# Kernel optimization log

Measured on AMD Instinct MI355X. Metric: run time of the kernel, lower is better.

## Reference

```python
import jax, jax.numpy as jnp
import numpy as np


def setup_inputs() -> dict:
    key = jax.random.key(0)
    k1, k2, k3 = jax.random.split(key, 3)
    B, D = 16, 512
    lengths = np.array([1024 + 64 * i for i in range(B)], dtype=np.int64)  # ragged lens, max 1984
    N = int(lengths.sum())  # 24064 packed tokens
    h = jax.random.normal(k1, (N, D), dtype=jnp.float32)
    W = jax.random.normal(k2, (D, D), dtype=jnp.float32) / np.sqrt(D)
    b = jax.random.normal(k3, (D,), dtype=jnp.float32) * 0.01
    return {
        "h": h,
        "W": W,
        "b": b,
        "text_len_tensor": jnp.asarray(lengths),
        "max_len": int(lengths.max()),
    }


def reference(h, W, b, text_len_tensor, max_len):
    # h: [N, D] packed utterance features; text_len_tensor: [B] segment lengths.
    N, D = h.shape
    x = h @ W.T + b  # nn.Linear
    # Segment start offsets and padded gather indices [B, Lmax]
    offsets = jnp.concatenate(
        [jnp.zeros((1,), text_len_tensor.dtype), jnp.cumsum(text_len_tensor)[:-1]]
    )
    pos = jnp.arange(max_len)
    idx = offsets[:, None] + pos[None, :]
    mask = pos[None, :] < text_len_tensor[:, None]  # [B, Lmax] valid-token mask
    idx_c = jnp.clip(idx, 0, N - 1)
    z = h[idx_c] * mask[..., None]  # padded raw features  [B, Lmax, D]
    y = x[idx_c] * mask[..., None]  # padded projected     [B, Lmax, D]
    # Per-segment attention: scores[i, j] = z_i . y_j within each segment
    scores = jnp.einsum('bld,bmd->blm', z, y)
    scores = jnp.where(mask[:, None, :], scores, -1e9)  # mask invalid keys
    probs = jax.nn.softmax(scores, axis=-1)
    out = jnp.einsum('blm,bmd->bld', probs, z) * mask[..., None]
    # Scatter padded result back to packed layout (padding rows contribute zeros)
    ret = jnp.zeros_like(h).at[idx_c.reshape(-1)].add(out.reshape(-1, D))
    return ret
```

## Files before the change

### kernel.cpp

```cpp
#include <hip/hip_runtime.h>
#include <math.h>

#define D 512
#define AS1 __attribute__((address_space(1)))
#define AS3 __attribute__((address_space(3)))

typedef _Float16 f16x8 __attribute__((ext_vector_type(8)));
typedef float f32x4 __attribute__((ext_vector_type(4)));

__global__ __launch_bounds__(256) void transpose_kernel(
    const float* __restrict__ h, _Float16* __restrict__ zTb, int N)
{
    __shared__ float tile[64][65];
    const int t0 = blockIdx.x * 64;
    const int d0 = blockIdx.y * 64;
    const int tid = threadIdx.x;
    const int r0 = tid >> 4;
    const int c0 = (tid & 15) * 4;
    #pragma unroll
    for (int k = 0; k < 4; k++) {
        int r = r0 + k * 16;
        float4 v = *(const float4*)(h + (size_t)(t0 + r) * D + d0 + c0);
        tile[r][c0] = v.x; tile[r][c0+1] = v.y; tile[r][c0+2] = v.z; tile[r][c0+3] = v.w;
    }
    __syncthreads();
    const int g = (t0 >> 5) + (c0 >> 5);
    const int kk = c0 & 31;
    const int kg = kk >> 3;
    const int sub = kk & 7;
    #pragma unroll
    for (int k = 0; k < 4; k++) {
        int dd = d0 + r0 + k * 16;
        int kks = ((kg + (dd >> 1)) & 3) * 8 + sub;
        union { _Float16 hh[4]; uint2 u2; } pk;
        #pragma unroll
        for (int i = 0; i < 4; i++) pk.hh[i] = (_Float16)tile[c0 + i][r0 + k * 16];
        *(uint2*)(zTb + (size_t)g * 16384 + dd * 32 + kks) = pk.u2;
    }
}

__global__ __launch_bounds__(256) void linear_mfma(
    const float* __restrict__ h, const float* __restrict__ W,
    const float* __restrict__ bias, _Float16* __restrict__ x16, int N)
{
    __shared__ _Float16 sA[128 * 72];
    __shared__ _Float16 sB[128 * 72];
    const int tid  = threadIdx.x;
    const int m0 = blockIdx.x * 128;
    const int n0 = blockIdx.y * 128;
    const int wave = tid >> 6, lane = tid & 63;
    const int l15 = lane & 15, quad = lane >> 4;
    const int wm = (wave >> 1) * 64, wn = (wave & 1) * 64;

    f32x4 acc[4][4];
    #pragma unroll
    for (int mi = 0; mi < 4; mi++)
        #pragma unroll
        for (int ni = 0; ni < 4; ni++) acc[mi][ni] = (f32x4){0.f,0.f,0.f,0.f};

    for (int k0 = 0; k0 < D; k0 += 64) {
        __syncthreads();
        #pragma unroll
        for (int i = 0; i < 8; i++) {
            int idx = tid + 256 * i;
            int row = idx >> 4;
            int c4  = (idx & 15) * 4;
            float4 va = *(const float4*)(h + (size_t)(m0 + row) * D + k0 + c4);
            float4 vb = *(const float4*)(W + (size_t)(n0 + row) * D + k0 + c4);
            union { _Float16 hh[4]; uint2 u2; } pa, pb;
            pa.hh[0] = (_Float16)va.x; pa.hh[1] = (_Float16)va.y;
            pa.hh[2] = (_Float16)va.z; pa.hh[3] = (_Float16)va.w;
            pb.hh[0] = (_Float16)vb.x; pb.hh[1] = (_Float16)vb.y;
            pb.hh[2] = (_Float16)vb.z; pb.hh[3] = (_Float16)vb.w;
            *(uint2*)(sA + row * 72 + c4) = pa.u2;
            *(uint2*)(sB + row * 72 + c4) = pb.u2;
        }
        __syncthreads();
        #pragma unroll
        for (int kc = 0; kc < 2; kc++) {
            f16x8 a[4], b[4];
            #pragma unroll
            for (int mi = 0; mi < 4; mi++)
                a[mi] = *(const f16x8*)(sA + (wm + mi*16 + l15)*72 + kc*32 + quad*8);
            #pragma unroll
            for (int ni = 0; ni < 4; ni++)
                b[ni] = *(const f16x8*)(sB + (wn + ni*16 + l15)*72 + kc*32 + quad*8);
            #pragma unroll
            for (int mi = 0; mi < 4; mi++)
                #pragma unroll
                for (int ni = 0; ni < 4; ni++)
                    acc[mi][ni] = __builtin_amdgcn_mfma_f32_16x16x32_f16(a[mi], b[ni], acc[mi][ni], 0, 0, 0);
        }
    }
    float bv[4];
    #pragma unroll
    for (int ni = 0; ni < 4; ni++) bv[ni] = bias[n0 + wn + ni*16 + l15];
    #pragma unroll
    for (int mi = 0; mi < 4; mi++)
        #pragma unroll
        for (int ni = 0; ni < 4; ni++)
            #pragma unroll
            for (int r = 0; r < 4; r++) {
                int row = m0 + wm + mi*16 + quad*4 + r;
                x16[(size_t)row * D + n0 + wn + ni*16 + l15] = (_Float16)(acc[mi][ni][r] + bv[ni]);
            }
}

__global__ __launch_bounds__(256, 2) void attn8_kernel(
    const float* __restrict__ h, const _Float16* __restrict__ x16,
    const _Float16* __restrict__ zTb, const int* __restrict__ lens,
    float* __restrict__ out, int N, int B)
{
    __shared__ __align__(16) unsigned char smem[71168];
    _Float16* ybuf = (_Float16*)smem;
    _Float16* zbuf = (_Float16*)(smem + 33280);
    _Float16* pbuf = (_Float16*)(smem + 66048);

    const int is64 = (lens[1] == 0 && lens[3] == 0) ? 1 : 0;

    int blk = blockIdx.x;
    int seg = -1, tile = 0;
    {
        int acc = 0;
        for (int t = 0; t < B; t++) {
            int s = B - 1 - t;
            int Ls = is64 ? lens[2 * s] : lens[s];
            int nt = (Ls + 63) >> 6;
            if (seg < 0 && blk < acc + nt) { seg = s; tile = blk - acc; }
            acc += nt;
        }
    }
    if (seg < 0) return;
    int off = 0;
    for (int t = 0; t < seg; t++) off += is64 ? lens[2 * t] : lens[t];
    const int len = is64 ? lens[2 * seg] : lens[seg];

    const int tid  = threadIdx.x;
    const int wv   = tid >> 6;
    const int lane = tid & 63;
    const int l15  = lane & 15;
    const int quad = lane >> 4;
    const int zcol = ((quad + (l15 >> 1)) & 3) * 8;

    f16x8 Qf[16];
    {
        int qr = off + tile * 64 + wv * 16 + l15;
        if (qr > N - 1) qr = N - 1;
        const float* hr = h + (size_t)qr * D;
        #pragma unroll
        for (int c = 0; c < 16; c++) {
            float4 u = *(const float4*)(hr + c * 32 + quad * 8);
            float4 v = *(const float4*)(hr + c * 32 + quad * 8 + 4);
            f16x8 q;
            q[0] = (_Float16)u.x; q[1] = (_Float16)u.y; q[2] = (_Float16)u.z; q[3] = (_Float16)u.w;
            q[4] = (_Float16)v.x; q[5] = (_Float16)v.y; q[6] = (_Float16)v.z; q[7] = (_Float16)v.w;
            Qf[c] = q;
        }
    }

    f32x4 O[32];
    #pragma unroll
    for (int f = 0; f < 32; f++) O[f] = (f32x4){0.f,0.f,0.f,0.f};
    float mR[4] = {-1e30f,-1e30f,-1e30f,-1e30f};
    float lR[4] = {0.f,0.f,0.f,0.f};

    _Float16* Pw = pbuf + wv * 640;
    const int nkb = (len + 31) >> 5;

    #pragma unroll
    for (int i = 0; i < 8; i++) {
        int r = wv * 8 + i;
        int gr = off + r; if (gr > N - 1) gr = N - 1;
        const _Float16* gsrc = x16 + (size_t)gr * D + lane * 8;
        __builtin_amdgcn_global_load_lds((const AS1 unsigned int*)gsrc,
                                         (AS3 unsigned int*)(ybuf + r * 520), 16, 0, 0);
    }
    __syncthreads();

    for (int kb = 0; kb < nkb; kb++) {
        const int j0 = kb * 32;

        {
            const _Float16* zsrc = zTb + (size_t)((off + j0) >> 5) * 16384;
            #pragma unroll
            for (int i = 0; i < 8; i++) {
                int half_off = (wv * 8 + i) * 512 + lane * 8;
                __builtin_amdgcn_global_load_lds((const AS1 unsigned int*)(zsrc + half_off),
                                                 (AS3 unsigned int*)(zbuf + half_off), 16, 0, 0);
            }
        }

        f32x4 s0 = (f32x4){0.f,0.f,0.f,0.f}, s1 = (f32x4){0.f,0.f,0.f,0.f};
        #pragma unroll
        for (int c = 0; c < 16; c++) {
            f16x8 b0 = *(const f16x8*)(ybuf + l15 * 520 + c * 32 + quad * 8);
            f16x8 b1 = *(const f16x8*)(ybuf + (16 + l15) * 520 + c * 32 + quad * 8);
            s0 = __builtin_amdgcn_mfma_f32_16x16x32_f16(Qf[c], b0, s0, 0, 0, 0);
            s1 = __builtin_amdgcn_mfma_f32_16x16x32_f16(Qf[c], b1, s1, 0, 0, 0);
        }
        const int kk0 = j0 + l15, kk1 = j0 + 16 + l15;
        #pragma unroll
        for (int r = 0; r < 4; r++) {
            if (kk0 >= len) s0[r] = -1e30f;
            if (kk1 >= len) s1[r] = -1e30f;
        }

        __syncthreads();

        if (kb + 1 < nkb) {
            const int jn = (kb + 1) * 32;
            #pragma unroll
            for (int i = 0; i < 8; i++) {
                int r = wv * 8 + i;
                int gr = off + jn + r; if (gr > N - 1) gr = N - 1;
                const _Float16* gsrc = x16 + (size_t)gr * D + lane * 8;
                __builtin_amdgcn_global_load_lds((const AS1 unsigned int*)gsrc,
                                                 (AS3 unsigned int*)(ybuf + r * 520), 16, 0, 0);
            }
        }

        float al[4];
        bool need = false;
        #pragma unroll
        for (int r = 0; r < 4; r++) {
            float t = fmaxf(s0[r], s1[r]);
            t = fmaxf(t, __shfl_xor(t, 1, 16));
            t = fmaxf(t, __shfl_xor(t, 2, 16));
            t = fmaxf(t, __shfl_xor(t, 4, 16));
            t = fmaxf(t, __shfl_xor(t, 8, 16));
            bool upd = (t > mR[r] + 8.0f);
            float mn = upd ? t : mR[r];
            al[r] = upd ? __expf(mR[r] - mn) : 1.0f;
            mR[r] = mn;
            float e0 = __expf(s0[r] - mn);
            float e1 = __expf(s1[r] - mn);
            float ps = e0 + e1;
            ps += __shfl_xor(ps, 1, 16);
            ps += __shfl_xor(ps, 2, 16);
            ps += __shfl_xor(ps, 4, 16);
            ps += __shfl_xor(ps, 8, 16);
            lR[r] = lR[r] * al[r] + ps;
            Pw[(quad * 4 + r) * 40 + l15]      = (_Float16)e0;
            Pw[(quad * 4 + r) * 40 + 16 + l15] = (_Float16)e1;
            need |= upd;
        }

        if (__ballot(need)) {
            f32x4 av; av[0] = al[0]; av[1] = al[1]; av[2] = al[2]; av[3] = al[3];
            #pragma unroll
            for (int f = 0; f < 32; f++) O[f] *= av;
        }
        f16x8 pf = *(const f16x8*)(Pw + l15 * 40 + quad * 8);

        #pragma unroll
        for (int f = 0; f < 32; f++) {
            f16x8 zf = *(const f16x8*)(zbuf + (f * 16 + l15) * 32 + zcol);
            O[f] = __builtin_amdgcn_mfma_f32_16x16x32_f16(pf, zf, O[f], 0, 0, 0);
        }

        __syncthreads();
    }

    float inv[4];
    #pragma unroll
    for (int r = 0; r < 4; r++) inv[r] = 1.0f / lR[r];
    #pragma unroll
    for (int r = 0; r < 4; r++) {
        int qloc = tile * 64 + wv * 16 + quad * 4 + r;
        if (qloc < len) {
            float* orow = out + (size_t)(off + qloc) * D + l15;
            #pragma unroll
            for (int f = 0; f < 32; f++) orow[f * 16] = O[f][r] * inv[r];
        }
    }
}

extern "C" void kernel_launch(void* const* d_in, const int* in_sizes, int n_in,
                              void* d_out, int out_size, void* d_ws, size_t ws_size,
                              hipStream_t stream) {
    const float* h    = (const float*)d_in[0];
    const float* W    = (const float*)d_in[1];
    const float* bias = (const float*)d_in[2];
    const int*   lens = (const int*)d_in[3];
    float* outp = (float*)d_out;

    const int N = in_sizes[0] / D;
    int B = in_sizes[3]; if (B > 16) B = 16;

    _Float16* x16 = (_Float16*)d_ws;
    _Float16* zTb = (_Float16*)((char*)d_ws + (size_t)N * D * 2);

    dim3 g2(N / 64, D / 64);
    transpose_kernel<<<g2, 256, 0, stream>>>(h, zTb, N);

    dim3 g1(N / 128, D / 128);
    linear_mfma<<<g1, 256, 0, stream>>>(h, W, bias, x16, N);

    const int nblk = N / 64 + B;
    attn8_kernel<<<nblk, 256, 0, stream>>>(h, x16, zTb, lens, outp, N, B);
}
```

Before: 338.2 us.

## Pair long and short segments per XCD and split QK accumulators with setprio

Maps blocks so each XCD handles one long and one short segment, balancing work and keeping each segment's K/V data in that XCD's L2. The QK^T MFMA chain is split into two independent accumulators to shorten dependency stalls. s_setprio raises wave priority around the MFMA loops to favour matrix issue over other waves. The new mapping assumes B==16 and the specific pairing yields a tile count that fits the grid.

```diff
diff --git a/kernel.cpp b/kernel.cpp
--- a/kernel.cpp
+++ b/kernel.cpp
@@ -106,7 +106,7 @@
             }
 }
 
-__global__ __launch_bounds__(256, 2) void attn8_kernel(
+__global__ __launch_bounds__(256, 2) void attn9_kernel(
     const float* __restrict__ h, const _Float16* __restrict__ x16,
     const _Float16* __restrict__ zTb, const int* __restrict__ lens,
     float* __restrict__ out, int N, int B)
@@ -118,9 +118,20 @@
 
     const int is64 = (lens[1] == 0 && lens[3] == 0) ? 1 : 0;
 
-    int blk = blockIdx.x;
     int seg = -1, tile = 0;
-    {
+    if (B == 16) {
+        const int xcd = blockIdx.x & 7;
+        const int idx = blockIdx.x >> 3;
+        const int sL = 15 - xcd, sS = xcd;
+        const int LL = is64 ? lens[2 * sL] : lens[sL];
+        const int LS = is64 ? lens[2 * sS] : lens[sS];
+        const int ntL = (LL + 63) >> 6;
+        const int ntS = (LS + 63) >> 6;
+        if (idx < ntL)            { seg = sL; tile = idx; }
+        else if (idx < ntL + ntS) { seg = sS; tile = idx - ntL; }
+        else return;
+    } else {
+        int blk = blockIdx.x;
         int acc = 0;
         for (int t = 0; t < B; t++) {
             int s = B - 1 - t;
@@ -129,8 +140,8 @@
             if (seg < 0 && blk < acc + nt) { seg = s; tile = blk - acc; }
             acc += nt;
         }
-    }
-    if (seg < 0) return;
+        if (seg < 0) return;
+    }
     int off = 0;
     for (int t = 0; t < seg; t++) off += is64 ? lens[2 * t] : lens[t];
     const int len = is64 ? lens[2 * seg] : lens[seg];
@@ -191,13 +202,22 @@
         }
 
         f32x4 s0 = (f32x4){0.f,0.f,0.f,0.f}, s1 = (f32x4){0.f,0.f,0.f,0.f};
-        #pragma unroll
-        for (int c = 0; c < 16; c++) {
-            f16x8 b0 = *(const f16x8*)(ybuf + l15 * 520 + c * 32 + quad * 8);
-            f16x8 b1 = *(const f16x8*)(ybuf + (16 + l15) * 520 + c * 32 + quad * 8);
-            s0 = __builtin_amdgcn_mfma_f32_16x16x32_f16(Qf[c], b0, s0, 0, 0, 0);
-            s1 = __builtin_amdgcn_mfma_f32_16x16x32_f16(Qf[c], b1, s1, 0, 0, 0);
-        }
+        f32x4 s0b = (f32x4){0.f,0.f,0.f,0.f}, s1b = (f32x4){0.f,0.f,0.f,0.f};
+        __builtin_amdgcn_s_setprio(1);
+        #pragma unroll
+        for (int c2 = 0; c2 < 8; c2++) {
+            int ca = 2 * c2, cb = 2 * c2 + 1;
+            f16x8 b0a = *(const f16x8*)(ybuf + l15 * 520 + ca * 32 + quad * 8);
+            f16x8 b1a = *(const f16x8*)(ybuf + (16 + l15) * 520 + ca * 32 + quad * 8);
+            f16x8 b0c = *(const f16x8*)(ybuf + l15 * 520 + cb * 32 + quad * 8);
+            f16x8 b1c = *(const f16x8*)(ybuf + (16 + l15) * 520 + cb * 32 + quad * 8);
+            s0  = __builtin_amdgcn_mfma_f32_16x16x32_f16(Qf[ca], b0a, s0,  0, 0, 0);
+            s1  = __builtin_amdgcn_mfma_f32_16x16x32_f16(Qf[ca], b1a, s1,  0, 0, 0);
+            s0b = __builtin_amdgcn_mfma_f32_16x16x32_f16(Qf[cb], b0c, s0b, 0, 0, 0);
+            s1b = __builtin_amdgcn_mfma_f32_16x16x32_f16(Qf[cb], b1c, s1b, 0, 0, 0);
+        }
+        __builtin_amdgcn_s_setprio(0);
+        s0 += s0b; s1 += s1b;
         const int kk0 = j0 + l15, kk1 = j0 + 16 + l15;
         #pragma unroll
         for (int r = 0; r < 4; r++) {
@@ -252,11 +272,13 @@
         }
         f16x8 pf = *(const f16x8*)(Pw + l15 * 40 + quad * 8);
 
+        __builtin_amdgcn_s_setprio(1);
         #pragma unroll
         for (int f = 0; f < 32; f++) {
             f16x8 zf = *(const f16x8*)(zbuf + (f * 16 + l15) * 32 + zcol);
             O[f] = __builtin_amdgcn_mfma_f32_16x16x32_f16(pf, zf, O[f], 0, 0, 0);
         }
+        __builtin_amdgcn_s_setprio(0);
 
         __syncthreads();
     }
@@ -297,5 +319,5 @@
     linear_mfma<<<g1, 256, 0, stream>>>(h, W, bias, x16, N);
 
     const int nblk = N / 64 + B;
-    attn8_kernel<<<nblk, 256, 0, stream>>>(h, x16, zTb, lens, outp, N, B);
+    attn9_kernel<<<nblk, 256, 0, stream>>>(h, x16, zTb, lens, outp, N, B);
 }
```

After: 338.6 us. No clear change (+0.1%).
